# Kernel optimization log

Measured on AMD Instinct MI355X. Metric: run time of the kernel, lower is better.

The kernel has to match this reference:

```python
import jax, jax.numpy as jnp
import numpy as np

D = 256        # d_model
DL = 256       # d_latent
S = 2048       # seq_len
B = 8          # batches
F = 8192       # facts per batch (padded)
MAXPOS = 4096
MAXPRED = 1024
NROLE = 64 + 2 # role_emb rows


def setup_inputs() -> dict:
    key = jax.random.key(0)
    ks = jax.random.split(key, 16)
    def nrm(k, shape, s=0.02):
        return jax.random.normal(k, shape, jnp.float32) * s
    return {
        "pos_emb": nrm(ks[0], (MAXPOS, D)),
        "pred_emb": nrm(ks[1], (MAXPRED, D)),
        "role_emb": nrm(ks[2], (NROLE, D)),
        "w1": nrm(ks[3], (3 * D, 2 * D)), "b1": jnp.zeros((2 * D,), jnp.float32),
        "w2": nrm(ks[4], (2 * D, D)),     "b2": jnp.zeros((D,), jnp.float32),
        "ln_g": jnp.ones((D,), jnp.float32), "ln_b": jnp.zeros((D,), jnp.float32),
        "lw1": nrm(ks[5], (D, DL)), "lb1": jnp.zeros((DL,), jnp.float32),
        "lw2": nrm(ks[6], (DL, DL)), "lb2": jnp.zeros((DL,), jnp.float32),
        "pred_idx": jax.random.randint(ks[7], (B, F), 0, MAXPRED),
        "a0": jax.random.randint(ks[8], (B, F), 0, S),
        "a1": jax.random.randint(ks[9], (B, F), 0, S),
        "role_idx": jax.random.randint(ks[10], (B, F), 0, NROLE),
        "is_role": jax.random.randint(ks[11], (B, F), 0, 2).astype(jnp.int32),
        "add_rev": jax.random.randint(ks[12], (B, F), 0, 2).astype(jnp.int32),
        "mask": jax.random.randint(ks[13], (B, F), 0, 2).astype(jnp.int32),
        "seq_len": S,
    }


def reference(pos_emb, pred_emb, role_emb, w1, b1, w2, b2, ln_g, ln_b,
              lw1, lb1, lw2, lb2,
              pred_idx, a0, a1, role_idx, is_role, add_rev, mask, seq_len):
    nodes = pos_emb[:seq_len]                 # [S, D] shared across batches
    pe = pred_emb[pred_idx]                   # [B, F, D]
    n0 = nodes[a0]                            # [B, F, D]
    n1 = nodes[a1]                            # [B, F, D]
    re = role_emb[role_idx]                   # [B, F, D]

    role_b = is_role.astype(bool)
    valid = mask.astype(bool)

    third = jnp.where(role_b[..., None], re, n1)
    x_fwd = jnp.concatenate([n0, pe, third], axis=-1)   # [B, F, 3D]
    x_rev = jnp.concatenate([n1, pe, n0], axis=-1)      # [B, F, 3D]

    def mlp(x):
        h = jax.nn.gelu(x @ w1 + b1, approximate=False)
        return h @ w2 + b2

    msg_fwd = mlp(x_fwd)                      # [B, F, D]
    msg_rev = mlp(x_rev)                      # [B, F, D]

    w_fwd = valid[..., None].astype(msg_fwd.dtype)
    w_rev = (valid & (~role_b) & add_rev.astype(bool))[..., None].astype(msg_rev.dtype)
    tgt_fwd = jnp.where(role_b, a0, a1)       # role msgs go to tok=a0, binary to a1

    def scat(msg, idx, w):
        return jax.ops.segment_sum(msg * w, idx, num_segments=seq_len)

    agg = jax.vmap(scat)(msg_fwd, tgt_fwd, w_fwd)
    agg = agg + jax.vmap(scat)(msg_rev, a0, w_rev)      # [B, S, D]

    x = nodes[None, :, :] + agg
    mu = jnp.mean(x, axis=-1, keepdims=True)
    var = jnp.mean(jnp.square(x - mu), axis=-1, keepdims=True)
    x = (x - mu) / jnp.sqrt(var + 1e-5) * ln_g + ln_b   # LayerNorm

    pooled = jnp.mean(x, axis=1)              # [B, D]
    h = jax.nn.gelu(pooled @ lw1 + lb1, approximate=False)
    return h @ lw2 + lb2                      # [B, DL]
```

## Files before the change

kernel.cpp:

```cpp
#include <hip/hip_runtime.h>
#include <hip/hip_bf16.h>
#include <cstdint>

#define S_LEN 2048
#define DIM   256
#define NBAT  8
#define NEDGE 65536
#define HID   512
#define INDIM 768

#define OFF_AGG   0u
#define OFF_POOL  16777216u
#define OFF_CNT   16785408u
#define OFF_NODES 16785664u
#define OFF_PRED  17834240u
#define OFF_ROLE  18358528u
#define OFF_W1P   18392576u
#define OFF_W2P   19179008u
#define OFF_FWD   19441152u
#define OFF_REV   19703296u
#define ZERO_BYTES 16785664u

typedef short bshort8 __attribute__((ext_vector_type(8)));
typedef float floatx4 __attribute__((ext_vector_type(4)));
typedef ushort ushort4v __attribute__((ext_vector_type(4)));

__device__ __forceinline__ float gelu_f(float x) {
  return 0.5f * x * (1.0f + erff(x * 0.70710678118654752f));
}
__device__ __forceinline__ ushort f2bf(float v) {
  __hip_bfloat16 h = __float2bfloat16(v);
  return *reinterpret_cast<ushort*>(&h);
}

#define Z4 1049104
#define T4 200832
#define WN 524288
__global__ void prep_all(const float* __restrict__ pos, const float* __restrict__ pred,
                         const float* __restrict__ role,
                         const float* __restrict__ w1, const float* __restrict__ w2,
                         unsigned char* __restrict__ ws) {
  int i = blockIdx.x * blockDim.x + threadIdx.x;
  if (i < Z4) {
    reinterpret_cast<float4*>(ws)[i] = float4{0.f, 0.f, 0.f, 0.f};
    return;
  }
  i -= Z4;
  if (i < T4) {
    const int NN4 = 131072, NP4 = 65536;
    float4 v;
    if (i < NN4) v = reinterpret_cast<const float4*>(pos)[i];
    else if (i < NN4 + NP4) v = reinterpret_cast<const float4*>(pred)[i - NN4];
    else v = reinterpret_cast<const float4*>(role)[i - NN4 - NP4];
    ushort4v h;
    h.x = f2bf(v.x); h.y = f2bf(v.y); h.z = f2bf(v.z); h.w = f2bf(v.w);
    *reinterpret_cast<ushort4v*>((ushort*)(ws + OFF_NODES) + (i << 2)) = h;
    return;
  }
  i -= T4;
  if (i < WN) {
    ushort* W1p = (ushort*)(ws + OFF_W1P);
    ushort* W2p = (ushort*)(ws + OFF_W2P);
    const int N1 = INDIM * HID;
    if (i < N1) {
      int k = i >> 9, n = i & 511;
      W1p[(((k >> 3) << 9) + n) * 8 + (k & 7)] = f2bf(w1[i]);
    } else {
      int j = i - N1;
      int k = j >> 8, n = j & 255;
      W2p[(((k >> 3) << 8) + n) * 8 + (k & 7)] = f2bf(w2[j]);
    }
  }
}

__global__ void build_lists(const int* __restrict__ mask, const int* __restrict__ is_role,
                            const int* __restrict__ add_rev,
                            int* __restrict__ fwd, int* __restrict__ rev, int* __restrict__ cnt) {
  int e = blockIdx.x * blockDim.x + threadIdx.x;
  int lane = threadIdx.x & 63;
  bool c0 = mask[e] != 0;
  bool c1 = c0 && !is_role[e] && add_rev[e];
  unsigned long long b0 = __ballot(c0);
  unsigned long long b1m = __ballot(c1);
  unsigned long long lt = (1ull << lane) - 1ull;
  int base0 = 0, base1 = 0;
  if (lane == 0) {
    base0 = atomicAdd(&cnt[0], __popcll(b0));
    base1 = atomicAdd(&cnt[1], __popcll(b1m));
  }
  base0 = __shfl(base0, 0);
  base1 = __shfl(base1, 0);
  if (c0) fwd[base0 + __popcll(b0 & lt)] = e;
  if (c1) rev[base1 + __popcll(b1m & lt)] = e;
}

#define HSTR_E 520
__global__ __launch_bounds__(512, 4)
void mlp_kernel(const int* __restrict__ cnt, const int* __restrict__ fwd, const int* __restrict__ rev,
                const int* __restrict__ a0, const int* __restrict__ a1,
                const int* __restrict__ pred_idx, const int* __restrict__ role_idx,
                const int* __restrict__ is_role,
                const ushort* __restrict__ T,
                const ushort* __restrict__ W1p, const ushort* __restrict__ W2p,
                const float* __restrict__ b1, const float* __restrict__ b2,
                float* __restrict__ agg) {
  __shared__ ushort Hs[64 * HSTR_E];
  __shared__ int ltgt[64];
  __shared__ int lbat[64];
  __shared__ uint loff[64][3];

  const int tid = threadIdx.x;
  const int nf = cnt[0], nr = cnt[1];
  const int total = nf + nr;
  const int row0 = blockIdx.x * 64;
  if (row0 >= total) return;

  if (tid < 64) {
    int grow = row0 + tid;
    int tgt = -1, bb = 0; uint o0 = 0, o1 = 0, o2 = 0;
    if (grow < total) {
      bool rv = grow >= nf;
      int e = rv ? rev[grow - nf] : fwd[grow];
      bb = e >> 13;
      int A0 = a0[e], A1 = a1[e];
      o1 = 524288u + ((uint)pred_idx[e] << 8);
      if (rv)              { o0 = (uint)A1 << 8; o2 = (uint)A0 << 8;                      tgt = A0; }
      else if (is_role[e]) { o0 = (uint)A0 << 8; o2 = 786432u + ((uint)role_idx[e] << 8); tgt = A0; }
      else                 { o0 = (uint)A0 << 8; o2 = (uint)A1 << 8;                      tgt = A1; }
    }
    ltgt[tid] = tgt; lbat[tid] = bb;
    loff[tid][0] = o0; loff[tid][1] = o1; loff[tid][2] = o2;
  }
  __syncthreads();

  const int lane = tid & 63, wave = tid >> 6;
  const int wm = wave >> 2, wn = wave & 3;
  const int l15 = lane & 15, kb = lane >> 4;
  const int m0 = wm * 32 + l15;
  const int m1 = m0 + 16;

  const uint o00 = loff[m0][0], o01 = loff[m0][1], o02 = loff[m0][2];
  const uint o10 = loff[m1][0], o11 = loff[m1][1], o12 = loff[m1][2];

  floatx4 acc1[2][8];
#pragma unroll
  for (int fm = 0; fm < 2; ++fm)
#pragma unroll
    for (int fn = 0; fn < 8; ++fn) acc1[fm][fn] = (floatx4){0.f, 0.f, 0.f, 0.f};

  const int kcb = kb * 8;
  bshort8 xb0 = *reinterpret_cast<const bshort8*>(T + o00 + kcb);
  bshort8 xb1 = *reinterpret_cast<const bshort8*>(T + o10 + kcb);
#pragma unroll 1
  for (int k0 = 0; k0 < INDIM; k0 += 32) {
    int k1 = k0 + 32;
    uint po0 = (k1 < 256) ? o00 : (k1 < 512) ? o01 : o02;
    uint po1 = (k1 < 256) ? o10 : (k1 < 512) ? o11 : o12;
    int kc1 = (k1 & 255) + kcb;
    bshort8 nx0 = *reinterpret_cast<const bshort8*>(T + po0 + kc1);
    bshort8 nx1 = *reinterpret_cast<const bshort8*>(T + po1 + kc1);

    const ushort* wp = W1p + ((((k0 >> 3) + kb) << 9) + wn * 128 + l15) * 8;
#pragma unroll
    for (int fn = 0; fn < 8; ++fn) {
      bshort8 wv = *reinterpret_cast<const bshort8*>(wp + (fn << 7));
      acc1[0][fn] = __builtin_amdgcn_mfma_f32_16x16x32_bf16(wv, xb0, acc1[0][fn], 0, 0, 0);
      acc1[1][fn] = __builtin_amdgcn_mfma_f32_16x16x32_bf16(wv, xb1, acc1[1][fn], 0, 0, 0);
    }
    xb0 = nx0; xb1 = nx1;
  }

#pragma unroll
  for (int fm = 0; fm < 2; ++fm) {
    int m = fm ? m1 : m0;
#pragma unroll
    for (int fn = 0; fn < 8; ++fn) {
      int n0 = wn * 128 + fn * 16 + kb * 4;
      float4 bb4 = *reinterpret_cast<const float4*>(b1 + n0);
      ushort4v hv;
      hv.x = f2bf(gelu_f(acc1[fm][fn][0] + bb4.x));
      hv.y = f2bf(gelu_f(acc1[fm][fn][1] + bb4.y));
      hv.z = f2bf(gelu_f(acc1[fm][fn][2] + bb4.z));
      hv.w = f2bf(gelu_f(acc1[fm][fn][3] + bb4.w));
      *reinterpret_cast<ushort4v*>(Hs + m * HSTR_E + n0) = hv;
    }
  }
  __syncthreads();

  floatx4 acc2[2][4];
#pragma unroll
  for (int fm = 0; fm < 2; ++fm)
#pragma unroll
    for (int fn = 0; fn < 4; ++fn) acc2[fm][fn] = (floatx4){0.f, 0.f, 0.f, 0.f};

#pragma unroll 1
  for (int k0 = 0; k0 < HID; k0 += 32) {
    bshort8 ha0 = *reinterpret_cast<const bshort8*>(Hs + m0 * HSTR_E + k0 + kcb);
    bshort8 ha1 = *reinterpret_cast<const bshort8*>(Hs + m1 * HSTR_E + k0 + kcb);
    const ushort* wp2 = W2p + ((((k0 >> 3) + kb) << 8) + wn * 64 + l15) * 8;
#pragma unroll
    for (int fn = 0; fn < 4; ++fn) {
      bshort8 wv = *reinterpret_cast<const bshort8*>(wp2 + (fn << 7));
      acc2[0][fn] = __builtin_amdgcn_mfma_f32_16x16x32_bf16(ha0, wv, acc2[0][fn], 0, 0, 0);
      acc2[1][fn] = __builtin_amdgcn_mfma_f32_16x16x32_bf16(ha1, wv, acc2[1][fn], 0, 0, 0);
    }
  }

#pragma unroll
  for (int fn = 0; fn < 4; ++fn) {
    int n = wn * 64 + fn * 16 + l15;
    float bias = b2[n];
#pragma unroll
    for (int fm = 0; fm < 2; ++fm) {
#pragma unroll
      for (int rg = 0; rg < 4; ++rg) {
        int m = wm * 32 + fm * 16 + kb * 4 + rg;
        int tgt = ltgt[m];
        if (tgt >= 0) {
          unsafeAtomicAdd(agg + ((((uint)lbat[m] << 11) + (uint)tgt) << 8) + n,
                          acc2[fm][fn][rg] + bias);
        }
      }
    }
  }
}

__global__ void ln_pool(const float* __restrict__ pos, const float* __restrict__ agg,
                        const float* __restrict__ g, const float* __restrict__ be,
                        float* __restrict__ pooled_sum) {
  __shared__ float r2[16];
  const int b = blockIdx.x >> 7;
  const int sb = blockIdx.x & 127;
  const int t = threadIdx.x;
  const float gg = g[t], bb = be[t];
  const int wv = t >> 6;
  float psum = 0.f;
#pragma unroll 1
  for (int i = 0; i < 16; ++i) {
    int s = sb * 16 + i;
    float x = pos[s * DIM + t] + agg[((b << 11) + s) * DIM + t];
    float a = x, q = x * x;
#pragma unroll
    for (int o = 32; o > 0; o >>= 1) { a += __shfl_xor(a, o); q += __shfl_xor(q, o); }
    if ((t & 63) == 0) { r2[wv * 2] = a; r2[wv * 2 + 1] = q; }
    __syncthreads();
    a = r2[0] + r2[2] + r2[4] + r2[6];
    q = r2[1] + r2[3] + r2[5] + r2[7];
    __syncthreads();
    float mu = a * (1.f / 256.f);
    float var = q * (1.f / 256.f) - mu * mu;
    float y = (x - mu) * rsqrtf(var + 1e-5f) * gg + bb;
    psum += y;
  }
  unsafeAtomicAdd(&pooled_sum[(b << 8) + t], psum);
}

__global__ void final_mlp(const float* __restrict__ pooled_sum,
                          const float* __restrict__ lw1, const float* __restrict__ lb1,
                          const float* __restrict__ lw2, const float* __restrict__ lb2,
                          float* __restrict__ out) {
  __shared__ float pl[256];
  __shared__ float hl[256];
  const int r = blockIdx.x, t = threadIdx.x;
  pl[t] = pooled_sum[(r << 8) + t] * (1.f / 2048.f);
  __syncthreads();
  float a = lb1[t];
#pragma unroll 8
  for (int d = 0; d < 256; ++d) a = fmaf(pl[d], lw1[(d << 8) + t], a);
  hl[t] = gelu_f(a);
  __syncthreads();
  float o = lb2[t];
#pragma unroll 8
  for (int d = 0; d < 256; ++d) o = fmaf(hl[d], lw2[(d << 8) + t], o);
  out[(r << 8) + t] = o;
}

extern "C" void kernel_launch(void* const* d_in, const int* in_sizes, int n_in,
                              void* d_out, int out_size, void* d_ws, size_t ws_size,
                              hipStream_t stream) {
  const float* pos_emb  = (const float*)d_in[0];
  const float* pred_emb = (const float*)d_in[1];
  const float* role_emb = (const float*)d_in[2];
  const float* w1   = (const float*)d_in[3];
  const float* b1   = (const float*)d_in[4];
  const float* w2   = (const float*)d_in[5];
  const float* b2   = (const float*)d_in[6];
  const float* ln_g = (const float*)d_in[7];
  const float* ln_b = (const float*)d_in[8];
  const float* lw1  = (const float*)d_in[9];
  const float* lb1  = (const float*)d_in[10];
  const float* lw2  = (const float*)d_in[11];
  const float* lb2  = (const float*)d_in[12];
  const int* pred_idx = (const int*)d_in[13];
  const int* a0       = (const int*)d_in[14];
  const int* a1       = (const int*)d_in[15];
  const int* role_idx = (const int*)d_in[16];
  const int* is_role  = (const int*)d_in[17];
  const int* add_rev  = (const int*)d_in[18];
  const int* mask     = (const int*)d_in[19];

  unsigned char* ws = (unsigned char*)d_ws;
  float*  agg    = (float*)(ws + OFF_AGG);
  float*  pooled = (float*)(ws + OFF_POOL);
  int*    cnt    = (int*)(ws + OFF_CNT);
  ushort* T      = (ushort*)(ws + OFF_NODES);
  ushort* W1p    = (ushort*)(ws + OFF_W1P);
  ushort* W2p    = (ushort*)(ws + OFF_W2P);
  int*    fwd    = (int*)(ws + OFF_FWD);
  int*    rev    = (int*)(ws + OFF_REV);

  prep_all<<<6931, 256, 0, stream>>>(pos_emb, pred_emb, role_emb, w1, w2, ws);
  build_lists<<<256, 256, 0, stream>>>(mask, is_role, add_rev, fwd, rev, cnt);
  mlp_kernel<<<2048, 512, 0, stream>>>(cnt, fwd, rev, a0, a1, pred_idx, role_idx, is_role,
                                       T, W1p, W2p, b1, b2, agg);
  ln_pool<<<1024, 256, 0, stream>>>(pos_emb, agg, ln_g, ln_b, pooled);
  final_mlp<<<8, 256, 0, stream>>>(pooled, lw1, lb1, lw2, lb2, (float*)d_out);
}
```

Measured before the change: 289.9 us.

## Fuse list build into prep, split MLP hidden in halves, fuse final MLP

Merges the edge-list compaction into the prep kernel, with per-block atomics replacing per-wave ones, and zeroes the counters with a memset. The MLP kernel now computes the hidden layer in two 256-wide halves, which shrinks the LDS staging buffer and the accumulator registers and should help occupancy, at the cost of re-reading the gathered inputs twice. The final small MLP is folded into the LayerNorm/pool kernel through a last-block-done counter, saving a launch. The last block then runs the tail MLP serially on its own.

```diff
diff --git a/kernel.cpp b/kernel.cpp
--- a/kernel.cpp
+++ b/kernel.cpp
@@ -19,7 +19,6 @@
 #define OFF_W2P   19179008u
 #define OFF_FWD   19441152u
 #define OFF_REV   19703296u
-#define ZERO_BYTES 16785664u
 
 typedef short bshort8 __attribute__((ext_vector_type(8)));
 typedef float floatx4 __attribute__((ext_vector_type(4)));
@@ -33,14 +32,44 @@
   return *reinterpret_cast<ushort*>(&h);
 }
 
-#define Z4 1049104
+#define Z4 1049088
 #define T4 200832
 #define WN 524288
-__global__ void prep_all(const float* __restrict__ pos, const float* __restrict__ pred,
-                         const float* __restrict__ role,
-                         const float* __restrict__ w1, const float* __restrict__ w2,
-                         unsigned char* __restrict__ ws) {
-  int i = blockIdx.x * blockDim.x + threadIdx.x;
+#define FLAT_BLOCKS 6931
+__global__ void prep_build(const float* __restrict__ pos, const float* __restrict__ pred,
+                           const float* __restrict__ role,
+                           const float* __restrict__ w1, const float* __restrict__ w2,
+                           const int* __restrict__ mask, const int* __restrict__ is_role,
+                           const int* __restrict__ add_rev,
+                           unsigned char* __restrict__ ws) {
+  if (blockIdx.x >= FLAT_BLOCKS) {
+    __shared__ int wc0[4], wc1[4], base[2];
+    int* fwd = (int*)(ws + OFF_FWD);
+    int* rev = (int*)(ws + OFF_REV);
+    int* cnt = (int*)(ws + OFF_CNT);
+    int tid = threadIdx.x;
+    int e = (blockIdx.x - FLAT_BLOCKS) * 256 + tid;
+    int lane = tid & 63, w = tid >> 6;
+    bool c0 = mask[e] != 0;
+    bool c1 = c0 && !is_role[e] && add_rev[e];
+    unsigned long long b0 = __ballot(c0);
+    unsigned long long b1m = __ballot(c1);
+    unsigned long long lt = (1ull << lane) - 1ull;
+    if (lane == 0) { wc0[w] = __popcll(b0); wc1[w] = __popcll(b1m); }
+    __syncthreads();
+    if (tid == 0) {
+      base[0] = atomicAdd(&cnt[0], wc0[0] + wc0[1] + wc0[2] + wc0[3]);
+      base[1] = atomicAdd(&cnt[1], wc1[0] + wc1[1] + wc1[2] + wc1[3]);
+    }
+    __syncthreads();
+    int p0 = base[0], p1 = base[1];
+    for (int ww = 0; ww < 4; ++ww)
+      if (ww < w) { p0 += wc0[ww]; p1 += wc1[ww]; }
+    if (c0) fwd[p0 + __popcll(b0 & lt)] = e;
+    if (c1) rev[p1 + __popcll(b1m & lt)] = e;
+    return;
+  }
+  int i = blockIdx.x * 256 + threadIdx.x;
   if (i < Z4) {
     reinterpret_cast<float4*>(ws)[i] = float4{0.f, 0.f, 0.f, 0.f};
     return;
@@ -73,28 +102,7 @@
   }
 }
 
-__global__ void build_lists(const int* __restrict__ mask, const int* __restrict__ is_role,
-                            const int* __restrict__ add_rev,
-                            int* __restrict__ fwd, int* __restrict__ rev, int* __restrict__ cnt) {
-  int e = blockIdx.x * blockDim.x + threadIdx.x;
-  int lane = threadIdx.x & 63;
-  bool c0 = mask[e] != 0;
-  bool c1 = c0 && !is_role[e] && add_rev[e];
-  unsigned long long b0 = __ballot(c0);
-  unsigned long long b1m = __ballot(c1);
-  unsigned long long lt = (1ull << lane) - 1ull;
-  int base0 = 0, base1 = 0;
-  if (lane == 0) {
-    base0 = atomicAdd(&cnt[0], __popcll(b0));
-    base1 = atomicAdd(&cnt[1], __popcll(b1m));
-  }
-  base0 = __shfl(base0, 0);
-  base1 = __shfl(base1, 0);
-  if (c0) fwd[base0 + __popcll(b0 & lt)] = e;
-  if (c1) rev[base1 + __popcll(b1m & lt)] = e;
-}
-
-#define HSTR_E 520
+#define HSTR2 264
 __global__ __launch_bounds__(512, 4)
 void mlp_kernel(const int* __restrict__ cnt, const int* __restrict__ fwd, const int* __restrict__ rev,
                 const int* __restrict__ a0, const int* __restrict__ a1,
@@ -104,7 +112,7 @@
                 const ushort* __restrict__ W1p, const ushort* __restrict__ W2p,
                 const float* __restrict__ b1, const float* __restrict__ b2,
                 float* __restrict__ agg) {
-  __shared__ ushort Hs[64 * HSTR_E];
+  __shared__ ushort Hs[64 * HSTR2];
   __shared__ int ltgt[64];
   __shared__ int lbat[64];
   __shared__ uint loff[64][3];
@@ -136,74 +144,82 @@
   const int lane = tid & 63, wave = tid >> 6;
   const int wm = wave >> 2, wn = wave & 3;
   const int l15 = lane & 15, kb = lane >> 4;
+  const int kcb = kb * 8;
   const int m0 = wm * 32 + l15;
   const int m1 = m0 + 16;
 
   const uint o00 = loff[m0][0], o01 = loff[m0][1], o02 = loff[m0][2];
   const uint o10 = loff[m1][0], o11 = loff[m1][1], o12 = loff[m1][2];
 
-  floatx4 acc1[2][8];
+  floatx4 acc2[2][4];
 #pragma unroll
   for (int fm = 0; fm < 2; ++fm)
 #pragma unroll
-    for (int fn = 0; fn < 8; ++fn) acc1[fm][fn] = (floatx4){0.f, 0.f, 0.f, 0.f};
-
-  const int kcb = kb * 8;
-  bshort8 xb0 = *reinterpret_cast<const bshort8*>(T + o00 + kcb);
-  bshort8 xb1 = *reinterpret_cast<const bshort8*>(T + o10 + kcb);
+    for (int fn = 0; fn < 4; ++fn) acc2[fm][fn] = (floatx4){0.f, 0.f, 0.f, 0.f};
+
 #pragma unroll 1
-  for (int k0 = 0; k0 < INDIM; k0 += 32) {
-    int k1 = k0 + 32;
-    uint po0 = (k1 < 256) ? o00 : (k1 < 512) ? o01 : o02;
-    uint po1 = (k1 < 256) ? o10 : (k1 < 512) ? o11 : o12;
-    int kc1 = (k1 & 255) + kcb;
-    bshort8 nx0 = *reinterpret_cast<const bshort8*>(T + po0 + kc1);
-    bshort8 nx1 = *reinterpret_cast<const bshort8*>(T + po1 + kc1);
-
-    const ushort* wp = W1p + ((((k0 >> 3) + kb) << 9) + wn * 128 + l15) * 8;
-#pragma unroll
-    for (int fn = 0; fn < 8; ++fn) {
-      bshort8 wv = *reinterpret_cast<const bshort8*>(wp + (fn << 7));
-      acc1[0][fn] = __builtin_amdgcn_mfma_f32_16x16x32_bf16(wv, xb0, acc1[0][fn], 0, 0, 0);
-      acc1[1][fn] = __builtin_amdgcn_mfma_f32_16x16x32_bf16(wv, xb1, acc1[1][fn], 0, 0, 0);
-    }
-    xb0 = nx0; xb1 = nx1;
-  }
-
-#pragma unroll
-  for (int fm = 0; fm < 2; ++fm) {
-    int m = fm ? m1 : m0;
-#pragma unroll
-    for (int fn = 0; fn < 8; ++fn) {
-      int n0 = wn * 128 + fn * 16 + kb * 4;
-      float4 bb4 = *reinterpret_cast<const float4*>(b1 + n0);
-      ushort4v hv;
-      hv.x = f2bf(gelu_f(acc1[fm][fn][0] + bb4.x));
-      hv.y = f2bf(gelu_f(acc1[fm][fn][1] + bb4.y));
-      hv.z = f2bf(gelu_f(acc1[fm][fn][2] + bb4.z));
-      hv.w = f2bf(gelu_f(acc1[fm][fn][3] + bb4.w));
-      *reinterpret_cast<ushort4v*>(Hs + m * HSTR_E + n0) = hv;
-    }
-  }
-  __syncthreads();
-
-  floatx4 acc2[2][4];
-#pragma unroll
-  for (int fm = 0; fm < 2; ++fm)
-#pragma unroll
-    for (int fn = 0; fn < 4; ++fn) acc2[fm][fn] = (floatx4){0.f, 0.f, 0.f, 0.f};
-
+  for (int h = 0; h < 2; ++h) {
+    const int nb = h * 256 + wn * 64;
+
+    floatx4 acc1[2][4];
+#pragma unroll
+    for (int fm = 0; fm < 2; ++fm)
+#pragma unroll
+      for (int fn = 0; fn < 4; ++fn) acc1[fm][fn] = (floatx4){0.f, 0.f, 0.f, 0.f};
+
+    bshort8 xb0 = *reinterpret_cast<const bshort8*>(T + o00 + kcb);
+    bshort8 xb1 = *reinterpret_cast<const bshort8*>(T + o10 + kcb);
 #pragma unroll 1
-  for (int k0 = 0; k0 < HID; k0 += 32) {
-    bshort8 ha0 = *reinterpret_cast<const bshort8*>(Hs + m0 * HSTR_E + k0 + kcb);
-    bshort8 ha1 = *reinterpret_cast<const bshort8*>(Hs + m1 * HSTR_E + k0 + kcb);
-    const ushort* wp2 = W2p + ((((k0 >> 3) + kb) << 8) + wn * 64 + l15) * 8;
-#pragma unroll
-    for (int fn = 0; fn < 4; ++fn) {
-      bshort8 wv = *reinterpret_cast<const bshort8*>(wp2 + (fn << 7));
-      acc2[0][fn] = __builtin_amdgcn_mfma_f32_16x16x32_bf16(ha0, wv, acc2[0][fn], 0, 0, 0);
-      acc2[1][fn] = __builtin_amdgcn_mfma_f32_16x16x32_bf16(ha1, wv, acc2[1][fn], 0, 0, 0);
-    }
+    for (int k0 = 0; k0 < INDIM; k0 += 32) {
+      int k1 = k0 + 32;
+      uint po0 = (k1 < 256) ? o00 : (k1 < 512) ? o01 : o02;
+      uint po1 = (k1 < 256) ? o10 : (k1 < 512) ? o11 : o12;
+      int kc1 = (k1 & 255) + kcb;
+      bshort8 nx0 = *reinterpret_cast<const bshort8*>(T + po0 + kc1);
+      bshort8 nx1 = *reinterpret_cast<const bshort8*>(T + po1 + kc1);
+
+      const ushort* wp = W1p + ((((k0 >> 3) + kb) << 9) + nb + l15) * 8;
+#pragma unroll
+      for (int fn = 0; fn < 4; ++fn) {
+        bshort8 wv = *reinterpret_cast<const bshort8*>(wp + (fn << 7));
+        acc1[0][fn] = __builtin_amdgcn_mfma_f32_16x16x32_bf16(wv, xb0, acc1[0][fn], 0, 0, 0);
+        acc1[1][fn] = __builtin_amdgcn_mfma_f32_16x16x32_bf16(wv, xb1, acc1[1][fn], 0, 0, 0);
+      }
+      xb0 = nx0; xb1 = nx1;
+    }
+
+#pragma unroll
+    for (int fm = 0; fm < 2; ++fm) {
+      int m = fm ? m1 : m0;
+#pragma unroll
+      for (int fn = 0; fn < 4; ++fn) {
+        int nl = wn * 64 + fn * 16 + kb * 4;
+        float4 bb4 = *reinterpret_cast<const float4*>(b1 + nb + fn * 16 + kb * 4);
+        floatx4 a = fm ? acc1[1][fn] : acc1[0][fn];
+        ushort4v hv;
+        hv.x = f2bf(gelu_f(a[0] + bb4.x));
+        hv.y = f2bf(gelu_f(a[1] + bb4.y));
+        hv.z = f2bf(gelu_f(a[2] + bb4.z));
+        hv.w = f2bf(gelu_f(a[3] + bb4.w));
+        *reinterpret_cast<ushort4v*>(Hs + m * HSTR2 + nl) = hv;
+      }
+    }
+    __syncthreads();
+
+#pragma unroll 1
+    for (int kl = 0; kl < 256; kl += 32) {
+      bshort8 ha0 = *reinterpret_cast<const bshort8*>(Hs + m0 * HSTR2 + kl + kcb);
+      bshort8 ha1 = *reinterpret_cast<const bshort8*>(Hs + m1 * HSTR2 + kl + kcb);
+      int kg = h * 256 + kl;
+      const ushort* wp2 = W2p + ((((kg >> 3) + kb) << 8) + wn * 64 + l15) * 8;
+#pragma unroll
+      for (int fn = 0; fn < 4; ++fn) {
+        bshort8 wv = *reinterpret_cast<const bshort8*>(wp2 + (fn << 7));
+        acc2[0][fn] = __builtin_amdgcn_mfma_f32_16x16x32_bf16(ha0, wv, acc2[0][fn], 0, 0, 0);
+        acc2[1][fn] = __builtin_amdgcn_mfma_f32_16x16x32_bf16(ha1, wv, acc2[1][fn], 0, 0, 0);
+      }
+    }
+    __syncthreads();
   }
 
 #pragma unroll
@@ -225,10 +241,16 @@
   }
 }
 
-__global__ void ln_pool(const float* __restrict__ pos, const float* __restrict__ agg,
-                        const float* __restrict__ g, const float* __restrict__ be,
-                        float* __restrict__ pooled_sum) {
+__global__ void ln_pool_final(const float* __restrict__ pos, const float* __restrict__ agg,
+                              const float* __restrict__ g, const float* __restrict__ be,
+                              float* __restrict__ pooled_sum, int* __restrict__ cnt,
+                              const float* __restrict__ lw1, const float* __restrict__ lb1,
+                              const float* __restrict__ lw2, const float* __restrict__ lb2,
+                              float* __restrict__ out) {
   __shared__ float r2[16];
+  __shared__ int s_old;
+  __shared__ float pl[8 * 256];
+  __shared__ float hl[8 * 256];
   const int b = blockIdx.x >> 7;
   const int sb = blockIdx.x & 127;
   const int t = threadIdx.x;
@@ -253,26 +275,37 @@
     psum += y;
   }
   unsafeAtomicAdd(&pooled_sum[(b << 8) + t], psum);
-}
-
-__global__ void final_mlp(const float* __restrict__ pooled_sum,
-                          const float* __restrict__ lw1, const float* __restrict__ lb1,
-                          const float* __restrict__ lw2, const float* __restrict__ lb2,
-                          float* __restrict__ out) {
-  __shared__ float pl[256];
-  __shared__ float hl[256];
-  const int r = blockIdx.x, t = threadIdx.x;
-  pl[t] = pooled_sum[(r << 8) + t] * (1.f / 2048.f);
-  __syncthreads();
-  float a = lb1[t];
-#pragma unroll 8
-  for (int d = 0; d < 256; ++d) a = fmaf(pl[d], lw1[(d << 8) + t], a);
-  hl[t] = gelu_f(a);
-  __syncthreads();
-  float o = lb2[t];
-#pragma unroll 8
-  for (int d = 0; d < 256; ++d) o = fmaf(hl[d], lw2[(d << 8) + t], o);
-  out[(r << 8) + t] = o;
+  __syncthreads();
+  if (t == 0) {
+    __threadfence();
+    s_old = atomicAdd(&cnt[2], 1);
+  }
+  __syncthreads();
+  if (s_old != 1023) return;
+
+  for (int i = t; i < 2048; i += 256)
+    pl[i] = atomicAdd(&pooled_sum[i], 0.0f) * (1.f / 2048.f);
+  __syncthreads();
+  float acc[8];
+#pragma unroll
+  for (int r = 0; r < 8; ++r) acc[r] = lb1[t];
+  for (int d = 0; d < 256; ++d) {
+    float w = lw1[(d << 8) + t];
+#pragma unroll
+    for (int r = 0; r < 8; ++r) acc[r] = fmaf(pl[(r << 8) + d], w, acc[r]);
+  }
+#pragma unroll
+  for (int r = 0; r < 8; ++r) hl[(r << 8) + t] = gelu_f(acc[r]);
+  __syncthreads();
+#pragma unroll
+  for (int r = 0; r < 8; ++r) acc[r] = lb2[t];
+  for (int d = 0; d < 256; ++d) {
+    float w = lw2[(d << 8) + t];
+#pragma unroll
+    for (int r = 0; r < 8; ++r) acc[r] = fmaf(hl[(r << 8) + d], w, acc[r]);
+  }
+#pragma unroll
+  for (int r = 0; r < 8; ++r) out[(r << 8) + t] = acc[r];
 }
 
 extern "C" void kernel_launch(void* const* d_in, const int* in_sizes, int n_in,
@@ -309,10 +342,11 @@
   int*    fwd    = (int*)(ws + OFF_FWD);
   int*    rev    = (int*)(ws + OFF_REV);
 
-  prep_all<<<6931, 256, 0, stream>>>(pos_emb, pred_emb, role_emb, w1, w2, ws);
-  build_lists<<<256, 256, 0, stream>>>(mask, is_role, add_rev, fwd, rev, cnt);
+  hipMemsetAsync(ws + OFF_CNT, 0, 64, stream);
+  prep_build<<<FLAT_BLOCKS + 256, 256, 0, stream>>>(pos_emb, pred_emb, role_emb, w1, w2,
+                                                    mask, is_role, add_rev, ws);
   mlp_kernel<<<2048, 512, 0, stream>>>(cnt, fwd, rev, a0, a1, pred_idx, role_idx, is_role,
                                        T, W1p, W2p, b1, b2, agg);
-  ln_pool<<<1024, 256, 0, stream>>>(pos_emb, agg, ln_g, ln_b, pooled);
-  final_mlp<<<8, 256, 0, stream>>>(pooled, lw1, lb1, lw2, lb2, (float*)d_out);
-}
+  ln_pool_final<<<1024, 256, 0, stream>>>(pos_emb, agg, ln_g, ln_b, pooled, cnt,
+                                          lw1, lb1, lw2, lb2, (float*)d_out);
+}
```

After: 310.6 us. 7.1% more time.
